# Kernel tuning notes

Hardware: AMD Instinct MI355X
Metric: run time of the kernel (lower is better)

## Reference

```python
import jax, jax.numpy as jnp
import numpy as np

B, D, H, S = 32, 512, 256, 131072
CAP_LIMIT, MIN_NOV, STORE_TH, ACT_TH = 0.85, 0.4, 0.35, 0.5
STAB_TARGET = 0.1

def _lin(x, w, b):
    return x @ w.T + b

def _ln(x, g, b):
    m = x.mean(-1, keepdims=True)
    v = ((x - m) ** 2).mean(-1, keepdims=True)
    return (x - m) / jnp.sqrt(v + 1e-5) * g + b

def _l2n(x):
    return x / jnp.clip(jnp.linalg.norm(x, axis=-1, keepdims=True), 1e-12)

def _forward(new_content, query, memory_bank, access_times,
             rel_w1, rel_b1, rel_g, rel_bb, rel_w2, rel_b2,
             nov_w, nov_b, gate_w, gate_b,
             lru_w, lru_b, conf_w, conf_b, eg_w, eg_b,
             dd_w1, dd_b1, dd_w2, dd_b2,
             ds_w1, ds_b1, ds_w2, ds_b2,
             decay_rate, memory_change_ema, current_step):
    step = jnp.float32(current_step)
    mem0 = memory_bank
    capacity = jnp.float32((jnp.linalg.norm(mem0, axis=-1) > ACT_TH).sum()) / S
    # ---- store gating ----
    combined = jnp.concatenate([new_content, query], axis=-1)                 # [B, 2D]
    rel = jax.nn.relu(_lin(jax.nn.relu(_ln(_lin(combined, rel_w1, rel_b1), rel_g, rel_bb)), rel_w2, rel_b2))
    sims = _l2n(new_content) @ _l2n(mem0).T                                   # [B, S]
    max_sim = sims.max(axis=-1, keepdims=True)
    novelty = (1.0 - max_sim) / 2.0
    nov_feat = jax.nn.sigmoid(_lin(new_content, nov_w, nov_b))
    store_score = jax.nn.sigmoid(_lin(rel + nov_feat, gate_w, gate_b))        # [B,1]
    base_store = store_score.mean() > STORE_TH
    novelty_ok = novelty.mean() > MIN_NOV
    should_store = jnp.logical_and(base_store, novelty_ok)
    over_cap = capacity > CAP_LIMIT
    # ---- emergency erase (applied only when over capacity) ----
    age = jnp.maximum(step - access_times, 0.0)
    erase_sc0 = age / (age.max() + 1e-6) + (1.0 - jax.nn.sigmoid(jnp.linalg.norm(mem0, axis=-1)))
    victim = jnp.argmax(erase_sc0)
    mem = mem0.at[victim].set(jnp.where(over_cap, 0.0, mem0[victim]))
    at = access_times.at[victim].set(jnp.where(over_cap, -99999.0, access_times[victim]))
    # ---- learned erase scores ----
    lru = jax.nn.relu(_lin(((step - at) / 1000.0)[:, None], lru_w, lru_b))    # [S, 32]
    conf = jax.nn.sigmoid(_lin(mem, conf_w, conf_b))                          # [S, 32]
    erase_scores = jax.nn.sigmoid(_lin(jnp.concatenate([lru, conf], -1), eg_w, eg_b))[:, 0]
    # ---- conflict detection + drift (sequential masked scatter, faithful order) ----
    sims2 = _l2n(new_content) @ _l2n(mem).T                                   # [B, S]
    topv, topi = jax.lax.top_k(sims2, 3)                                      # [B, 3]
    conflict_mask = jnp.logical_and(topv > 0.7, topv < 0.99)
    old = mem[topi]                                                           # [B, 3, D]
    newb = jnp.broadcast_to(new_content[:, None, :], (B, 3, D))
    pair = jnp.concatenate([newb, old], axis=-1)                              # [B, 3, 2D]
    prob = jax.nn.sigmoid(_lin(jax.nn.relu(_lin(pair, dd_w1, dd_b1)), dd_w2, dd_b2))[..., 0]
    strength = jax.nn.sigmoid(_lin(jax.nn.relu(_lin(pair, ds_w1, ds_b1)), ds_w2, ds_b2))
    avg = (newb + old) / 2.0
    cand_new = (1.0 - strength) * newb + strength * avg
    cand_old = (1.0 - strength) * old + strength * avg
    active = jnp.logical_and(conflict_mask, prob > 0.5).reshape(-1)           # [B*3]
    fi = topi.reshape(-1)
    fn = cand_new.reshape(B * 3, D)
    fo = cand_old.reshape(B * 3, D)
    def body(i, carry):
        dn, do = carry
        b = i // 3
        s = fi[i]
        dn = dn.at[b].set(jnp.where(active[i], fn[i], dn[b]))
        do = do.at[s].set(jnp.where(active[i], fo[i], do[s]))
        return dn, do
    drifted_new, mem = jax.lax.fori_loop(0, B * 3, body, (new_content, mem))
    # ---- conditional store (no-grad write in original) ----
    write_idx = jnp.where(over_cap, victim, jnp.argmax(erase_scores))
    mem = mem.at[write_idx].set(jnp.where(should_store, jax.lax.stop_gradient(drifted_new[0]), mem[write_idx]))
    at = at.at[write_idx].set(jnp.where(should_store, step, at[write_idx]))
    # ---- stability / plasticity decay update ----
    change = jnp.abs(mem - mem0).mean()
    ema_new = 0.9 * memory_change_ema + 0.1 * change
    adjustment = jnp.where(ema_new.sum() > STAB_TARGET, -0.005, 0.005)
    decay_new = jnp.clip(decay_rate + adjustment, 0.01, 0.2)
    relevance = jax.nn.sigmoid(max_sim).mean()
    return (mem, at, erase_scores, store_score.mean(), novelty.mean(), relevance,
            capacity, conflict_mask.sum().astype(jnp.float32), decay_new, ema_new)

def setup_inputs() -> dict:
    key = jax.random.key(0)
    ks = iter(jax.random.split(key, 40))
    def rn(*shape):
        return jax.random.normal(next(ks), shape, dtype=jnp.float32) * 0.02
    return dict(
        new_content=jax.random.normal(next(ks), (B, D), dtype=jnp.float32),
        query=jax.random.normal(next(ks), (B, D), dtype=jnp.float32),
        memory_bank=jax.random.normal(next(ks), (S, D), dtype=jnp.float32),
        access_times=jax.random.uniform(next(ks), (S,), dtype=jnp.float32) * 1000.0,
        rel_w1=rn(H, 2 * D), rel_b1=jnp.zeros((H,)), rel_g=jnp.ones((H,)), rel_bb=jnp.zeros((H,)),
        rel_w2=rn(H // 2, H), rel_b2=jnp.zeros((H // 2,)),
        nov_w=rn(H // 2, D), nov_b=jnp.zeros((H // 2,)),
        gate_w=rn(1, H // 2), gate_b=jnp.zeros((1,)),
        lru_w=rn(32, 1), lru_b=jnp.zeros((32,)),
        conf_w=rn(32, D), conf_b=jnp.zeros((32,)),
        eg_w=rn(1, 64), eg_b=jnp.zeros((1,)),
        dd_w1=rn(H, 2 * D), dd_b1=jnp.zeros((H,)), dd_w2=rn(1, H), dd_b2=jnp.zeros((1,)),
        ds_w1=rn(H, 2 * D), ds_b1=jnp.zeros((H,)), ds_w2=rn(1, H), ds_b2=jnp.zeros((1,)),
        decay_rate=jnp.float32(0.04),
        memory_change_ema=jnp.zeros((1,), dtype=jnp.float32),
        current_step=5000,
    )

def reference(new_content, query, memory_bank, access_times,
              rel_w1, rel_b1, rel_g, rel_bb, rel_w2, rel_b2,
              nov_w, nov_b, gate_w, gate_b,
              lru_w, lru_b, conf_w, conf_b, eg_w, eg_b,
              dd_w1, dd_b1, dd_w2, dd_b2,
              ds_w1, ds_b1, ds_w2, ds_b2,
              decay_rate, memory_change_ema, current_step):
    return _forward(new_content, query, memory_bank, access_times,
                    rel_w1, rel_b1, rel_g, rel_bb, rel_w2, rel_b2,
                    nov_w, nov_b, gate_w, gate_b,
                    lru_w, lru_b, conf_w, conf_b, eg_w, eg_b,
                    dd_w1, dd_b1, dd_w2, dd_b2,
                    ds_w1, ds_b1, ds_w2, ds_b2,
                    decay_rate, memory_change_ema, current_step)
```

## Files before the change

### kernel.cpp

```cpp
#include <hip/hip_runtime.h>
#include <math.h>

typedef unsigned int u32;
typedef unsigned long long u64;

#define S_N 131072
#define OUT_AT   67108864L
#define OUT_ES   67239936L
#define OUT_SC   67371008L

#define W_WCT   0L
#define W_NORM2 32768L
#define W_CER   163840L
#define W_T4V   294912L
#define W_T4I   557056L
#define W_ATOM  819200L
#define W_FLAG  819208L
#define W_T3V   819216L
#define W_T3I   819312L
#define W_MAXS  819408L
#define W_ACT   819440L
#define W_CN    819536L
#define W_CO    868688L

__device__ __forceinline__ float sigm(float x){ return 1.0f/(1.0f + expf(-x)); }

__global__ __launch_bounds__(256) void k0(
    const float* __restrict__ nc, const float* __restrict__ query,
    const float* __restrict__ at_in,
    const float* __restrict__ rel_w1, const float* __restrict__ rel_b1,
    const float* __restrict__ rel_g, const float* __restrict__ rel_bb,
    const float* __restrict__ rel_w2, const float* __restrict__ rel_b2,
    const float* __restrict__ nov_w, const float* __restrict__ nov_b,
    const float* __restrict__ gate_w, const float* __restrict__ gate_b,
    const float* __restrict__ conf_w,
    const int* __restrict__ stepp,
    float* __restrict__ ws)
{
  const int bid = blockIdx.x, t = threadIdx.x;
  if (bid < 32) {
    __shared__ __align__(16) float scomb[1024];
    __shared__ __align__(16) float shr[256];
    __shared__ float red[256];
    const float* ncb = nc + bid*512;
    const float* qb  = query + bid*512;
    for (int i=t;i<1024;i+=256) scomb[i] = (i<512)? ncb[i] : qb[i-512];
    __syncthreads();
    float p = scomb[t]*scomb[t] + scomb[t+256]*scomb[t+256];
    red[t]=p; __syncthreads();
    for (int o=128;o>0;o>>=1){ if(t<o) red[t]+=red[t+o]; __syncthreads(); }
    const float denom = fmaxf(sqrtf(red[0]), 1e-12f);
    __syncthreads();
    float* wct = ws + W_WCT;
    wct[(long)t*64 + bid]       = scomb[t]/denom;
    wct[(long)(t+256)*64 + bid] = scomb[t+256]/denom;
    const float4* w1r = (const float4*)(rel_w1 + (long)t*1024);
    const float4* sc4 = (const float4*)scomb;
    float a1 = rel_b1[t];
    #pragma unroll 4
    for (int k=0;k<256;k++){ float4 w=w1r[k], s=sc4[k]; a1 += w.x*s.x+w.y*s.y+w.z*s.z+w.w*s.w; }
    red[t]=a1; __syncthreads();
    for (int o=128;o>0;o>>=1){ if(t<o) red[t]+=red[t+o]; __syncthreads(); }
    const float mean = red[0]/256.0f;
    __syncthreads();
    const float dd = a1-mean;
    red[t]=dd*dd; __syncthreads();
    for (int o=128;o>0;o>>=1){ if(t<o) red[t]+=red[t+o]; __syncthreads(); }
    const float var = red[0]/256.0f;
    __syncthreads();
    const float xh = (a1-mean)/sqrtf(var+1e-5f);
    shr[t] = fmaxf(xh*rel_g[t]+rel_bb[t], 0.0f);
    __syncthreads();
    float gp = 0.0f;
    if (t<128){
      const float4* w2r = (const float4*)(rel_w2 + (long)t*256);
      const float4* sh4 = (const float4*)shr;
      float a2 = rel_b2[t];
      #pragma unroll 4
      for (int k=0;k<64;k++){ float4 w=w2r[k], s=sh4[k]; a2 += w.x*s.x+w.y*s.y+w.z*s.z+w.w*s.w; }
      const float relv = fmaxf(a2,0.0f);
      const float4* nwr = (const float4*)(nov_w + (long)t*512);
      float a3 = nov_b[t];
      #pragma unroll 4
      for (int k=0;k<128;k++){ float4 w=nwr[k], s=sc4[k]; a3 += w.x*s.x+w.y*s.y+w.z*s.z+w.w*s.w; }
      gp = (relv + sigm(a3))*gate_w[t];
    }
    red[t]=gp; __syncthreads();
    for (int o=128;o>0;o>>=1){ if(t<o) red[t]+=red[t+o]; __syncthreads(); }
    if (t==0) atomicAdd((float*)(ws+W_ATOM+6), sigm(red[0]+gate_b[0]));
  } else if (bid < 64) {
    const int j = bid-32;
    float* wct = ws + W_WCT;
    for (int k=t;k<512;k+=256) wct[(long)k*64 + 32 + j] = conf_w[j*512+k];
  } else {
    __shared__ float red[256];
    const float step = (float)(*stepp);
    const int per = (S_N + 191)/192;
    const int base = (bid-64)*per;
    const int end = min(base+per, S_N);
    float m = 0.0f;
    for (int s=base+t; s<end; s+=256) m = fmaxf(m, fmaxf(step - at_in[s], 0.0f));
    red[t]=m; __syncthreads();
    for (int o=128;o>0;o>>=1){ if(t<o) red[t]=fmaxf(red[t],red[t+o]); __syncthreads(); }
    if (t==0) atomicMax((u32*)(ws+W_ATOM+0), __float_as_uint(red[0]));
  }
}

__global__ __launch_bounds__(256,3) void k1(
    const float* __restrict__ mem,
    const float* __restrict__ conf_b, const float* __restrict__ eg_w,
    float* __restrict__ out, float* __restrict__ ws)
{
  __shared__ __align__(16) float SM[8768];
  float* const lx = SM;
  float* const lw = SM + 4352;
  float* const ssim  = SM;
  float* const snorm = SM + 2112;

  const int t = threadIdx.x, bid = blockIdx.x;
  const long rowbase = (long)bid*64;
  const int lane = t & 63;
  const int hr = t >> 4;
  const int cj = t & 15;
  const int c4 = cj*4;
  const int q = t & 3, c16 = (t>>2)&3, r4 = t>>4;
  const int swz = r4 & 3;
  const float* wct = ws + W_WCT;

  float acc[4][16];
  #pragma unroll
  for (int i=0;i<4;i++){
    #pragma unroll
    for (int m=0;m<16;m++) acc[i][m]=0.0f;
  }
  float normp[4] = {0.0f,0.0f,0.0f,0.0f};
  float4 xv[4];

  #pragma unroll
  for (int it=0;it<4;++it)
    xv[it] = *(const float4*)(mem + (rowbase + 16*it + hr)*512 + c4);

  #pragma unroll 1
  for (int ch=0; ch<8; ++ch){
    #pragma unroll
    for (int it=0;it<4;++it){
      const int r = 16*it + hr;
      float4 v = xv[it];
      *(float4*)(out + (rowbase + r)*512 + ch*64 + c4) = v;
      normp[it] += v.x*v.x + v.y*v.y + v.z*v.z + v.w*v.w;
      *(float4*)&lx[r*68 + (cj ^ ((r>>2)&3))*4] = v;
    }
    #pragma unroll
    for (int it=0;it<4;++it){
      float4 w = *(const float4*)(wct + (long)(ch*64 + 16*it + hr)*64 + c4);
      *(float4*)&lw[hr*276 + it*68 + c4] = w;
    }
    __syncthreads();
    if (ch<7){
      #pragma unroll
      for (int it=0;it<4;++it)
        xv[it] = *(const float4*)(mem + (rowbase + 16*it + hr)*512 + (ch+1)*64 + c4);
    }
    #pragma unroll
    for (int kk4=0; kk4<4; ++kk4) {
      float xa[4][4];
      #pragma unroll
      for (int i=0;i<4;i++){
        float4 v = *(const float4*)&lx[(r4*4+i)*68 + (((q*4+kk4)^swz)*4)];
        xa[i][0]=v.x; xa[i][1]=v.y; xa[i][2]=v.z; xa[i][3]=v.w;
      }
      #pragma unroll
      for (int e=0;e<4;e++){
        const float* wp = &lw[(kk4*4+e)*276 + q*68 + c16*16];
        float4 w0 = *(const float4*)(wp);
        float4 w1 = *(const float4*)(wp+4);
        float4 w2 = *(const float4*)(wp+8);
        float4 w3 = *(const float4*)(wp+12);
        #pragma unroll
        for (int i=0;i<4;i++){
          const float xs = xa[i][e];
          acc[i][0]+=xs*w0.x; acc[i][1]+=xs*w0.y; acc[i][2]+=xs*w0.z; acc[i][3]+=xs*w0.w;
          acc[i][4]+=xs*w1.x; acc[i][5]+=xs*w1.y; acc[i][6]+=xs*w1.z; acc[i][7]+=xs*w1.w;
          acc[i][8]+=xs*w2.x; acc[i][9]+=xs*w2.y; acc[i][10]+=xs*w2.z; acc[i][11]+=xs*w2.w;
          acc[i][12]+=xs*w3.x; acc[i][13]+=xs*w3.y; acc[i][14]+=xs*w3.z; acc[i][15]+=xs*w3.w;
        }
      }
    }
    __syncthreads();
  }

  #pragma unroll
  for (int it=0; it<4; ++it) {
    float v = normp[it];
    v += __shfl_xor(v,8); v += __shfl_xor(v,4); v += __shfl_xor(v,2); v += __shfl_xor(v,1);
    if ((lane & 15)==0) snorm[16*it + hr] = v;
  }
  #pragma unroll
  for (int i=0;i<4;i++){
    #pragma unroll
    for (int m=0;m<16;m++){
      float v = acc[i][m];
      v += __shfl_xor(v,1);
      v += __shfl_xor(v,2);
      acc[i][m]=v;
    }
  }
  __syncthreads();
  if (q==0){
    if (c16<2){
      #pragma unroll
      for (int i=0;i<4;i++){
        const int R = r4*4+i;
        const float inv = 1.0f/fmaxf(sqrtf(snorm[R]),1e-12f);
        #pragma unroll
        for (int m=0;m<16;m++) ssim[R*33 + c16*16+m] = acc[i][m]*inv;
      }
    } else {
      #pragma unroll
      for (int i=0;i<4;i++){
        float part=0.0f;
        #pragma unroll
        for (int m=0;m<16;m++){
          const int j=(c16-2)*16+m;
          part += eg_w[32+j]*sigm(acc[i][m]+conf_b[j]);
        }
        part += __shfl_xor(part,4);
        if (c16==2) (ws+W_CER)[rowbase + r4*4+i]=part;
      }
    }
  }
  if (t<64) (ws+W_NORM2)[rowbase + t] = snorm[t];
  __syncthreads();
  if (t==0) {
    u32 c=0;
    for (int r=0;r<64;r++) c += (sqrtf(snorm[r]) > 0.5f)?1u:0u;
    atomicAdd((u32*)(ws+W_ATOM+1), c);
  }
  if (t<32) {
    float v0=-2,v1=-2,v2=-2,v3=-2; int i0=0,i1=0,i2=0,i3=0;
    for (int r=0;r<64;r++){
      const float v = ssim[r*33 + t]; const int gi = (int)rowbase + r;
      if (v > v2) {
        if (v > v0)      { v3=v2;i3=i2; v2=v1;i2=i1; v1=v0;i1=i0; v0=v;i0=gi; }
        else if (v > v1) { v3=v2;i3=i2; v2=v1;i2=i1; v1=v;i1=gi; }
        else             { v3=v2;i3=i2; v2=v;i2=gi; }
      } else if (v > v3) { v3=v;i3=gi; }
    }
    float* t4v = ws + W_T4V + (long)t*8192 + bid*4;
    int*   t4i = (int*)(ws + W_T4I) + (long)t*8192 + bid*4;
    t4v[0]=v0; t4v[1]=v1; t4v[2]=v2; t4v[3]=v3;
    t4i[0]=i0; t4i[1]=i1; t4i[2]=i2; t4i[3]=i3;
  }
}

__global__ __launch_bounds__(256) void kv2(
    const float* __restrict__ at_in, const int* __restrict__ stepp,
    float* __restrict__ ws, float* __restrict__ out)
{
  __shared__ u64 red[256];
  const int t = threadIdx.x, bid = blockIdx.x;
  if (bid==0 && t==0) {
    const u32 cnt = *(u32*)(ws+W_ATOM+1);
    const float cap = (float)cnt / (float)S_N;
    out[OUT_SC+3] = cap;
    ((int*)(ws+W_FLAG))[0] = (cap > 0.85f) ? 1 : 0;
  }
  const float step = (float)(*stepp);
  const float agemax = __uint_as_float(*(u32*)(ws+W_ATOM+0));
  const float dnm = agemax + 1e-6f;
  const float* n2 = ws+W_NORM2;
  const int base = bid*512;
  u64 best = 0;
  #pragma unroll
  for (int i=0;i<2;i++) {
    const int s = base + t + i*256;
    const float age = fmaxf(step - at_in[s], 0.0f);
    const float q = age/dnm;
    const float nr = sqrtf(n2[s]);
    const float sc = q + (1.0f - sigm(nr));
    const u64 key = ((u64)__float_as_uint(sc)<<32) | (u64)(0xFFFFFFFFu - (u32)s);
    best = (key>best)?key:best;
  }
  red[t]=best; __syncthreads();
  for (int o=128;o>0;o>>=1){ if(t<o){ u64 a=red[t],b2=red[t+o]; red[t]=(a>b2)?a:b2; } __syncthreads(); }
  if (t==0) atomicMax((u64*)(ws+W_ATOM+2), red[0]);
}

__device__ __forceinline__ void ins3(float v, int idx, float* V, int* I){
  if ( (v>V[0]) || (v==V[0] && idx<I[0]) ) { V[2]=V[1];I[2]=I[1]; V[1]=V[0];I[1]=I[0]; V[0]=v;I[0]=idx; }
  else if ( (v>V[1]) || (v==V[1] && idx<I[1]) ) { V[2]=V[1];I[2]=I[1]; V[1]=v;I[1]=idx; }
  else if ( (v>V[2]) || (v==V[2] && idx<I[2]) ) { V[2]=v;I[2]=idx; }
}

__global__ __launch_bounds__(256) void k3m(
    const float* __restrict__ at_in, const int* __restrict__ stepp,
    const float* __restrict__ lru_w, const float* __restrict__ lru_b,
    const float* __restrict__ eg_w, const float* __restrict__ eg_b,
    const float* __restrict__ conf_b,
    float* __restrict__ ws, float* __restrict__ out)
{
  __shared__ u64 red[256];
  __shared__ float lv[768];
  __shared__ int   li[768];
  __shared__ float lm[256];
  const int t=threadIdx.x, bid=blockIdx.x;
  const u64 vk = *(u64*)(ws+W_ATOM+2);
  const int victim = (int)(0xFFFFFFFFu - (u32)(vk & 0xFFFFFFFFull));
  const int oc = ((int*)(ws+W_FLAG))[0];
  if (bid < 256) {
    if (bid==0 && t==0) ((int*)(ws+W_FLAG))[1] = victim;
    const float step = (float)(*stepp);
    float* at_out = out + OUT_AT;
    float* es_out = out + OUT_ES;
    const float* cer = ws+W_CER;
    u64 best=0;
    const int base=bid*512;
    for (int i=0;i<2;i++){
      const int s = base + t + i*256;
      const float a = at_in[s];
      const bool isv = oc && (s==victim);
      const float av = isv ? -99999.0f : a;
      at_out[s] = av;
      const float x = (step - av)/1000.0f;
      float lsum = 0.0f;
      #pragma unroll
      for (int j=0;j<32;j++) lsum += eg_w[j]*fmaxf(lru_w[j]*x + lru_b[j], 0.0f);
      float ce;
      if (isv) { ce=0.0f; for (int j=0;j<32;j++) ce += eg_w[32+j]*sigm(conf_b[j]); }
      else ce = cer[s];
      const float es = sigm(lsum + ce + eg_b[0]);
      es_out[s] = es;
      const u64 key = ((u64)__float_as_uint(es)<<32) | (u64)(0xFFFFFFFFu - (u32)s);
      best = (key>best)?key:best;
    }
    red[t]=best; __syncthreads();
    for (int o=128;o>0;o>>=1){ if(t<o){ u64 a=red[t],b2=red[t+o]; red[t]=(a>b2)?a:b2; } __syncthreads(); }
    if (t==0) atomicMax((u64*)(ws+W_ATOM+4), red[0]);
  } else {
    const int b = bid - 256;
    const float* t4v = ws + W_T4V + (long)b*8192;
    const int*   t4i = (const int*)(ws + W_T4I) + (long)b*8192;
    float V[3] = {-2,-2,-2}; int I[3] = {0,0,0};
    float mx = -2.0f;
    for (int c=t; c<8192; c+=256) {
      const float v = t4v[c];
      const int idx = t4i[c];
      if ((c&3)==0) mx = fmaxf(mx, v);
      if (oc && idx==victim) continue;
      ins3(v, idx, V, I);
    }
    lv[t*3]=V[0]; lv[t*3+1]=V[1]; lv[t*3+2]=V[2];
    li[t*3]=I[0]; li[t*3+1]=I[1]; li[t*3+2]=I[2];
    lm[t]=mx;
    __syncthreads();
    for (int off=128; off>=1; off>>=1){
      if (t<off){
        float AV[3]={lv[t*3],lv[t*3+1],lv[t*3+2]};
        int   AI[3]={li[t*3],li[t*3+1],li[t*3+2]};
        ins3(lv[(t+off)*3+0], li[(t+off)*3+0], AV, AI);
        ins3(lv[(t+off)*3+1], li[(t+off)*3+1], AV, AI);
        ins3(lv[(t+off)*3+2], li[(t+off)*3+2], AV, AI);
        lv[t*3]=AV[0]; lv[t*3+1]=AV[1]; lv[t*3+2]=AV[2];
        li[t*3]=AI[0]; li[t*3+1]=AI[1]; li[t*3+2]=AI[2];
        lm[t]=fmaxf(lm[t], lm[t+off]);
      }
      __syncthreads();
    }
    if (t==0) {
      float FV[3]={lv[0],lv[1],lv[2]}; int FI[3]={li[0],li[1],li[2]};
      if (oc) ins3(0.0f, victim, FV, FI);
      for (int p=0;p<3;p++){ (ws+W_T3V)[b*3+p]=FV[p]; ((int*)(ws+W_T3I))[b*3+p]=FI[p]; }
      (ws+W_MAXS)[b]=lm[0];
    }
  }
}

__global__ __launch_bounds__(256) void k4(
    const float* __restrict__ mem, const float* __restrict__ nc,
    const float* __restrict__ dd_w1, const float* __restrict__ dd_b1,
    const float* __restrict__ dd_w2, const float* __restrict__ dd_b2,
    const float* __restrict__ ds_w1, const float* __restrict__ ds_b1,
    const float* __restrict__ ds_w2, const float* __restrict__ ds_b2,
    float* __restrict__ ws, float* __restrict__ out)
{
  const int bid = blockIdx.x, t = threadIdx.x;
  const int oc = ((int*)(ws+W_FLAG))[0];
  const int victim = ((int*)(ws+W_FLAG))[1];
  if (bid == 96) {
    if (t==0) {
      const float sm = (ws+W_ATOM)[6] / 32.0f;
      float nsum=0.0f, rsum=0.0f, csum=0.0f;
      for (int b2=0;b2<32;b2++){
        const float ms = (ws+W_MAXS)[b2];
        nsum += (1.0f-ms)/2.0f;
        rsum += sigm(ms);
      }
      for (int c=0;c<96;c++){
        const float v=(ws+W_T3V)[c];
        if (v>0.7f && v<0.99f) csum += 1.0f;
      }
      const float novm = nsum/32.0f;
      out[OUT_SC+0]=sm;
      out[OUT_SC+1]=novm;
      out[OUT_SC+2]=rsum/32.0f;
      out[OUT_SC+4]=csum;
      ((int*)(ws+W_FLAG))[2] = (sm>0.35f && novm>0.4f) ? 1 : 0;
      const u64 ek = *(u64*)(ws+W_ATOM+4);
      const int esidx = (int)(0xFFFFFFFFu - (u32)(ek & 0xFFFFFFFFull));
      ((int*)(ws+W_FLAG))[3] = oc ? victim : esidx;
    }
    return;
  }
  __shared__ __align__(16) float sp[1024];
  __shared__ __align__(16) float sh[256];
  __shared__ float red[256];
  const int b = bid/3;
  const int oi = ((int*)(ws+W_T3I))[bid];
  const float tv = (ws+W_T3V)[bid];
  const bool zold = oc && (oi==victim);
  for (int i=t;i<1024;i+=256)
    sp[i] = (i<512) ? nc[b*512+i] : (zold ? 0.0f : mem[(long)oi*512 + (i-512)]);
  __syncthreads();
  const float4* sp4 = (const float4*)sp;
  {
    const float4* wr = (const float4*)(dd_w1 + (long)t*1024);
    float a = dd_b1[t];
    #pragma unroll 4
    for (int k=0;k<256;k++){ float4 w=wr[k], s=sp4[k]; a += w.x*s.x+w.y*s.y+w.z*s.z+w.w*s.w; }
    sh[t]=fmaxf(a,0.0f);
  }
  __syncthreads();
  red[t]=sh[t]*dd_w2[t]; __syncthreads();
  for (int o=128;o>0;o>>=1){ if(t<o) red[t]+=red[t+o]; __syncthreads(); }
  const float prob = sigm(red[0]+dd_b2[0]);
  __syncthreads();
  {
    const float4* wr = (const float4*)(ds_w1 + (long)t*1024);
    float a = ds_b1[t];
    #pragma unroll 4
    for (int k=0;k<256;k++){ float4 w=wr[k], s=sp4[k]; a += w.x*s.x+w.y*s.y+w.z*s.z+w.w*s.w; }
    sh[t]=fmaxf(a,0.0f);
  }
  __syncthreads();
  red[t]=sh[t]*ds_w2[t]; __syncthreads();
  for (int o=128;o>0;o>>=1){ if(t<o) red[t]+=red[t+o]; __syncthreads(); }
  const float sstr = sigm(red[0]+ds_b2[0]);
  if (t==0) ((int*)(ws+W_ACT))[bid] = ((tv>0.7f) && (tv<0.99f) && (prob>0.5f)) ? 1 : 0;
  for (int k=t;k<512;k+=256){
    const float nw=sp[k], od=sp[512+k];
    const float avg=(nw+od)/2.0f;
    (ws+W_CN)[(long)bid*512+k] = (1.0f-sstr)*nw + sstr*avg;
    (ws+W_CO)[(long)bid*512+k] = (1.0f-sstr)*od + sstr*avg;
  }
}

__global__ __launch_bounds__(256) void k5(
    const float* __restrict__ mem, const float* __restrict__ nc,
    const float* __restrict__ decay_in, const float* __restrict__ ema_in,
    const int* __restrict__ stepp,
    float* __restrict__ ws, float* __restrict__ out)
{
  __shared__ int rows[256];
  __shared__ int nrows_s;
  __shared__ float red[256];
  const int t=threadIdx.x;
  const int oc=((int*)(ws+W_FLAG))[0];
  const int victim=((int*)(ws+W_FLAG))[1];
  const int should=((int*)(ws+W_FLAG))[2];
  const int widx=((int*)(ws+W_FLAG))[3];
  const int* act=(const int*)(ws+W_ACT);
  const int* t3i=(const int*)(ws+W_T3I);
  const float step=(float)(*stepp);
  float* at_out = out+OUT_AT;
  if (oc) { for (int k=t;k<512;k+=256) out[(long)victim*512+k]=0.0f; }
  __threadfence(); __syncthreads();
  for (int i=0;i<96;i++){
    if (act[i]) {
      const long s=t3i[i];
      for (int k=t;k<512;k+=256) out[s*512+k]=(ws+W_CO)[(long)i*512+k];
    }
  }
  int dn_src=-1;
  for (int i=0;i<3;i++) if (act[i]) dn_src=i;
  __threadfence(); __syncthreads();
  if (should) {
    for (int k=t;k<512;k+=256)
      out[(long)widx*512+k] = (dn_src>=0)? (ws+W_CN)[(long)dn_src*512+k] : nc[k];
    if (t==0) at_out[widx]=step;
  }
  __threadfence(); __syncthreads();
  if (t==0){
    int n=0;
    if (oc) rows[n++]=victim;
    for (int i=0;i<96;i++) if (act[i]) {
      const int s=t3i[i]; bool dup=false;
      for (int j=0;j<n;j++) if (rows[j]==s) dup=true;
      if (!dup) rows[n++]=s;
    }
    if (should) {
      bool dup=false;
      for (int j=0;j<n;j++) if (rows[j]==widx) dup=true;
      if (!dup) rows[n++]=widx;
    }
    nrows_s=n;
  }
  __syncthreads();
  float part=0.0f;
  for (int ri=0;ri<nrows_s;ri++){
    const long base=(long)rows[ri]*512;
    for (int k=t;k<512;k+=256) part += fabsf(out[base+k]-mem[base+k]);
  }
  red[t]=part; __syncthreads();
  for (int o=128;o>0;o>>=1){ if(t<o) red[t]+=red[t+o]; __syncthreads(); }
  if (t==0){
    const float change = red[0]/67108864.0f;
    const float ema = 0.9f*ema_in[0] + 0.1f*change;
    const float adj = (ema>0.1f)? -0.005f : 0.005f;
    const float dec = fminf(fmaxf(decay_in[0]+adj,0.01f),0.2f);
    out[OUT_SC+5]=dec;
    out[OUT_SC+6]=ema;
  }
}

extern "C" void kernel_launch(void* const* d_in, const int* in_sizes, int n_in,
                              void* d_out, int out_size, void* d_ws, size_t ws_size,
                              hipStream_t stream) {
  const float* nc     = (const float*)d_in[0];
  const float* query  = (const float*)d_in[1];
  const float* mem    = (const float*)d_in[2];
  const float* at_in  = (const float*)d_in[3];
  const float* rel_w1 = (const float*)d_in[4];
  const float* rel_b1 = (const float*)d_in[5];
  const float* rel_g  = (const float*)d_in[6];
  const float* rel_bb = (const float*)d_in[7];
  const float* rel_w2 = (const float*)d_in[8];
  const float* rel_b2 = (const float*)d_in[9];
  const float* nov_w  = (const float*)d_in[10];
  const float* nov_b  = (const float*)d_in[11];
  const float* gate_w = (const float*)d_in[12];
  const float* gate_b = (const float*)d_in[13];
  const float* lru_w  = (const float*)d_in[14];
  const float* lru_b  = (const float*)d_in[15];
  const float* conf_w = (const float*)d_in[16];
  const float* conf_b = (const float*)d_in[17];
  const float* eg_w   = (const float*)d_in[18];
  const float* eg_b   = (const float*)d_in[19];
  const float* dd_w1  = (const float*)d_in[20];
  const float* dd_b1  = (const float*)d_in[21];
  const float* dd_w2  = (const float*)d_in[22];
  const float* dd_b2  = (const float*)d_in[23];
  const float* ds_w1  = (const float*)d_in[24];
  const float* ds_b1  = (const float*)d_in[25];
  const float* ds_w2  = (const float*)d_in[26];
  const float* ds_b2  = (const float*)d_in[27];
  const float* decay  = (const float*)d_in[28];
  const float* ema    = (const float*)d_in[29];
  const int*   stepp  = (const int*)d_in[30];
  float* out = (float*)d_out;
  float* ws  = (float*)d_ws;

  hipMemsetAsync((char*)d_ws + (size_t)W_ATOM*4, 0, 32, stream);

  k0 <<<dim3(256), dim3(256), 0, stream>>>(nc, query, at_in, rel_w1, rel_b1, rel_g, rel_bb,
                                           rel_w2, rel_b2, nov_w, nov_b, gate_w, gate_b,
                                           conf_w, stepp, ws);
  k1 <<<dim3(2048), dim3(256), 0, stream>>>(mem, conf_b, eg_w, out, ws);
  kv2<<<dim3(256), dim3(256), 0, stream>>>(at_in, stepp, ws, out);
  k3m<<<dim3(288), dim3(256), 0, stream>>>(at_in, stepp, lru_w, lru_b, eg_w, eg_b, conf_b, ws, out);
  k4 <<<dim3(97),  dim3(256), 0, stream>>>(mem, nc, dd_w1, dd_b1, dd_w2, dd_b2,
                                           ds_w1, ds_b1, ds_w2, ds_b2, ws, out);
  k5 <<<dim3(1),   dim3(256), 0, stream>>>(mem, nc, decay, ema, stepp, ws, out);
}
```

Measured before the change: 420.6 us.

## Double-buffer memory-bank GEMM tiles via direct global-to-LDS loads and split out copy

The main similarity/confidence kernel now stages memory-bank and weight tiles straight into LDS using global_load_lds, with two buffers in flight and manual waitcnt/barrier control. This replaces the register-staged prefetch. Row norms are now accumulated from LDS reads, and the capacity count and norm stores are done per thread group instead of by a single thread. The copy of the 256MB memory bank to the output moves into a separate kernel. That frees the GEMM kernel from store traffic but reads the whole bank from HBM a second time.

Result: slower. 641.3 us (+52.5%).

```diff
diff --git a/kernel.cpp b/kernel.cpp
--- a/kernel.cpp
+++ b/kernel.cpp
@@ -106,26 +106,22 @@
   }
 }
 
-__global__ __launch_bounds__(256,3) void k1(
+__global__ __launch_bounds__(256,3) void kg(
     const float* __restrict__ mem,
     const float* __restrict__ conf_b, const float* __restrict__ eg_w,
-    float* __restrict__ out, float* __restrict__ ws)
+    float* __restrict__ ws)
 {
-  __shared__ __align__(16) float SM[8768];
-  float* const lx = SM;
-  float* const lw = SM + 4352;
-  float* const ssim  = SM;
-  float* const snorm = SM + 2112;
+  __shared__ __align__(16) float SM[16384];
+  float* const ssim = SM;
 
   const int t = threadIdx.x, bid = blockIdx.x;
   const long rowbase = (long)bid*64;
   const int lane = t & 63;
-  const int hr = t >> 4;
-  const int cj = t & 15;
-  const int c4 = cj*4;
+  const int wv = t >> 6;
   const int q = t & 3, c16 = (t>>2)&3, r4 = t>>4;
   const int swz = r4 & 3;
   const float* wct = ws + W_WCT;
+  const int o0 = (0^q)*4, o1 = (1^q)*4, o2 = (2^q)*4, o3 = (3^q)*4;
 
   float acc[4][16];
   #pragma unroll
@@ -134,51 +130,58 @@
     for (int m=0;m<16;m++) acc[i][m]=0.0f;
   }
   float normp[4] = {0.0f,0.0f,0.0f,0.0f};
-  float4 xv[4];
-
-  #pragma unroll
-  for (int it=0;it<4;++it)
-    xv[it] = *(const float4*)(mem + (rowbase + 16*it + hr)*512 + c4);
+
+  auto issue_stage = [&](int ch){
+    float* lxd = SM + (ch&1)*4096;
+    float* lwd = SM + 8192 + (ch&1)*4096;
+    #pragma unroll
+    for (int j=0;j<4;j++){
+      const int seg = wv*4 + j;
+      const int row = seg*4 + (lane>>4);
+      const int cjl = (lane&15) ^ ((row>>2)&3);
+      __builtin_amdgcn_global_load_lds(
+        (const __attribute__((address_space(1))) float*)(mem + (rowbase+row)*512 + ch*64 + cjl*4),
+        (__attribute__((address_space(3))) float*)(lxd + seg*256), 16, 0, 0);
+    }
+    #pragma unroll
+    for (int j=0;j<4;j++){
+      const int seg = wv*4 + j;
+      const int kl  = seg*4 + (lane>>4);
+      const int cjl = (lane&15) ^ ((kl>>4)&3);
+      __builtin_amdgcn_global_load_lds(
+        (const __attribute__((address_space(1))) float*)(wct + (long)(ch*64+kl)*64 + cjl*4),
+        (__attribute__((address_space(3))) float*)(lwd + seg*256), 16, 0, 0);
+    }
+  };
+
+  issue_stage(0);
+  issue_stage(1);
 
   #pragma unroll 1
   for (int ch=0; ch<8; ++ch){
+    if (ch<7) asm volatile("s_waitcnt vmcnt(8)\n\ts_barrier" ::: "memory");
+    else      asm volatile("s_waitcnt vmcnt(0)\n\ts_barrier" ::: "memory");
+    const float* lxb = SM + (ch&1)*4096;
+    const float* lwb = SM + 8192 + (ch&1)*4096;
     #pragma unroll
-    for (int it=0;it<4;++it){
-      const int r = 16*it + hr;
-      float4 v = xv[it];
-      *(float4*)(out + (rowbase + r)*512 + ch*64 + c4) = v;
-      normp[it] += v.x*v.x + v.y*v.y + v.z*v.z + v.w*v.w;
-      *(float4*)&lx[r*68 + (cj ^ ((r>>2)&3))*4] = v;
-    }
-    #pragma unroll
-    for (int it=0;it<4;++it){
-      float4 w = *(const float4*)(wct + (long)(ch*64 + 16*it + hr)*64 + c4);
-      *(float4*)&lw[hr*276 + it*68 + c4] = w;
-    }
-    __syncthreads();
-    if (ch<7){
-      #pragma unroll
-      for (int it=0;it<4;++it)
-        xv[it] = *(const float4*)(mem + (rowbase + 16*it + hr)*512 + (ch+1)*64 + c4);
-    }
-    #pragma unroll
-    for (int kk4=0; kk4<4; ++kk4) {
-      float xa[4][4];
+    for (int kk4=0; kk4<4; ++kk4){
+      float xaf[4][4];
       #pragma unroll
       for (int i=0;i<4;i++){
-        float4 v = *(const float4*)&lx[(r4*4+i)*68 + (((q*4+kk4)^swz)*4)];
-        xa[i][0]=v.x; xa[i][1]=v.y; xa[i][2]=v.z; xa[i][3]=v.w;
+        float4 v = *(const float4*)&lxb[(r4*4+i)*64 + (((q*4+kk4)^swz)*4)];
+        normp[i] += v.x*v.x + v.y*v.y + v.z*v.z + v.w*v.w;
+        xaf[i][0]=v.x; xaf[i][1]=v.y; xaf[i][2]=v.z; xaf[i][3]=v.w;
       }
       #pragma unroll
       for (int e=0;e<4;e++){
-        const float* wp = &lw[(kk4*4+e)*276 + q*68 + c16*16];
-        float4 w0 = *(const float4*)(wp);
-        float4 w1 = *(const float4*)(wp+4);
-        float4 w2 = *(const float4*)(wp+8);
-        float4 w3 = *(const float4*)(wp+12);
+        const float* wp = &lwb[(q*16 + kk4*4 + e)*64 + c16*16];
+        float4 w0 = *(const float4*)(wp + o0);
+        float4 w1 = *(const float4*)(wp + o1);
+        float4 w2 = *(const float4*)(wp + o2);
+        float4 w3 = *(const float4*)(wp + o3);
         #pragma unroll
         for (int i=0;i<4;i++){
-          const float xs = xa[i][e];
+          const float xs = xaf[i][e];
           acc[i][0]+=xs*w0.x; acc[i][1]+=xs*w0.y; acc[i][2]+=xs*w0.z; acc[i][3]+=xs*w0.w;
           acc[i][4]+=xs*w1.x; acc[i][5]+=xs*w1.y; acc[i][6]+=xs*w1.z; acc[i][7]+=xs*w1.w;
           acc[i][8]+=xs*w2.x; acc[i][9]+=xs*w2.y; acc[i][10]+=xs*w2.z; acc[i][11]+=xs*w2.w;
@@ -186,14 +189,16 @@
         }
       }
     }
-    __syncthreads();
+    asm volatile("s_waitcnt lgkmcnt(0)\n\ts_barrier" ::: "memory");
+    if (ch+2<8) issue_stage(ch+2);
   }
 
   #pragma unroll
-  for (int it=0; it<4; ++it) {
-    float v = normp[it];
-    v += __shfl_xor(v,8); v += __shfl_xor(v,4); v += __shfl_xor(v,2); v += __shfl_xor(v,1);
-    if ((lane & 15)==0) snorm[16*it + hr] = v;
+  for (int i=0;i<4;i++){
+    float v = normp[i];
+    v += __shfl_xor(v,1);
+    v += __shfl_xor(v,2);
+    normp[i]=v;
   }
   #pragma unroll
   for (int i=0;i<4;i++){
@@ -206,14 +211,35 @@
     }
   }
   __syncthreads();
+
   if (q==0){
-    if (c16<2){
+    if (c16==0){
+      u32 cc=0;
+      #pragma unroll
+      for (int i=0;i<4;i++){
+        (ws+W_NORM2)[rowbase + r4*4+i] = normp[i];
+        cc += (sqrtf(normp[i])>0.5f)?1u:0u;
+      }
+      u32 v=cc;
+      v += __shfl_xor(v,1); v += __shfl_xor(v,2); v += __shfl_xor(v,4);
+      v += __shfl_xor(v,8); v += __shfl_xor(v,16); v += __shfl_xor(v,32);
+      if (lane==0) atomicAdd((u32*)(ws+W_ATOM+1), v);
       #pragma unroll
       for (int i=0;i<4;i++){
         const int R = r4*4+i;
-        const float inv = 1.0f/fmaxf(sqrtf(snorm[R]),1e-12f);
+        const float inv = 1.0f/fmaxf(sqrtf(normp[i]),1e-12f);
         #pragma unroll
-        for (int m=0;m<16;m++) ssim[R*33 + c16*16+m] = acc[i][m]*inv;
+        for (int m=0;m<16;m++) ssim[R*33 + m] = acc[i][m]*inv;
+      }
+    } else if (c16==1){
+      u32 v=0;
+      (void)v;
+      #pragma unroll
+      for (int i=0;i<4;i++){
+        const int R = r4*4+i;
+        const float inv = 1.0f/fmaxf(sqrtf(normp[i]),1e-12f);
+        #pragma unroll
+        for (int m=0;m<16;m++) ssim[R*33 + 16 + m] = acc[i][m]*inv;
       }
     } else {
       #pragma unroll
@@ -229,13 +255,7 @@
       }
     }
   }
-  if (t<64) (ws+W_NORM2)[rowbase + t] = snorm[t];
   __syncthreads();
-  if (t==0) {
-    u32 c=0;
-    for (int r=0;r<64;r++) c += (sqrtf(snorm[r]) > 0.5f)?1u:0u;
-    atomicAdd((u32*)(ws+W_ATOM+1), c);
-  }
   if (t<32) {
     float v0=-2,v1=-2,v2=-2,v3=-2; int i0=0,i1=0,i2=0,i3=0;
     for (int r=0;r<64;r++){
@@ -251,6 +271,15 @@
     t4v[0]=v0; t4v[1]=v1; t4v[2]=v2; t4v[3]=v3;
     t4i[0]=i0; t4i[1]=i1; t4i[2]=i2; t4i[3]=i3;
   }
+}
+
+__global__ __launch_bounds__(256) void kcopy(const float* __restrict__ src, float* __restrict__ dst)
+{
+  const long i0 = (long)blockIdx.x*256 + threadIdx.x;
+  const float4* s4 = (const float4*)src;
+  float4* d4 = (float4*)dst;
+  #pragma unroll
+  for (int i=0;i<16;i++) d4[i0 + (long)i*1048576] = s4[i0 + (long)i*1048576];
 }
 
 __global__ __launch_bounds__(256) void kv2(
@@ -564,7 +593,8 @@
   k0 <<<dim3(256), dim3(256), 0, stream>>>(nc, query, at_in, rel_w1, rel_b1, rel_g, rel_bb,
                                            rel_w2, rel_b2, nov_w, nov_b, gate_w, gate_b,
                                            conf_w, stepp, ws);
-  k1 <<<dim3(2048), dim3(256), 0, stream>>>(mem, conf_b, eg_w, out, ws);
+  kg <<<dim3(2048), dim3(256), 0, stream>>>(mem, conf_b, eg_w, ws);
+  kcopy<<<dim3(4096), dim3(256), 0, stream>>>(mem, out);
   kv2<<<dim3(256), dim3(256), 0, stream>>>(at_in, stepp, ws, out);
   k3m<<<dim3(288), dim3(256), 0, stream>>>(at_in, stepp, lru_w, lru_b, eg_w, eg_b, conf_b, ws, out);
   k4 <<<dim3(97),  dim3(256), 0, stream>>>(mem, nc, dd_w1, dd_b1, dd_w2, dd_b2,
```
